# Kernel optimization log

Hardware: AMD Instinct MI355X
Metric: run time of the kernel (lower is better)

## Reference

```python
import jax, jax.numpy as jnp
import numpy as np

# Model dims (match init_kwargs)
B, S = 2, 2048          # batch, seq_len
H = 1024                # hidden_size
D = 2048                # expert_hidden_dim
E = 8                   # num_experts
K = 2                   # num_experts_per_tok (top_k)


def setup_inputs() -> dict:
    key = jax.random.key(0)
    k_x, k_g, k_w1, k_w2 = jax.random.split(key, 4)
    x = jax.random.normal(k_x, (B, S, H), jnp.float32)
    # router gate: Linear(H, E, bias=False)
    gate_w = jax.random.normal(k_g, (H, E), jnp.float32) / jnp.sqrt(H).astype(jnp.float32)
    # per-expert FFN params stacked on leading expert axis
    W1 = jax.random.normal(k_w1, (E, H, D), jnp.float32) / jnp.sqrt(H).astype(jnp.float32)
    b1 = jnp.zeros((E, D), jnp.float32)
    W2 = jax.random.normal(k_w2, (E, D, H), jnp.float32) / jnp.sqrt(D).astype(jnp.float32)
    b2 = jnp.zeros((E, H), jnp.float32)
    return {"x": x, "gate_w": gate_w, "W1": W1, "b1": b1, "W2": W2, "b2": b2}


def reference(x, gate_w, W1, b1, W2, b2):
    # --- router ---
    logits = jnp.einsum('bsh,he->bse', x, gate_w)            # [B,S,E]
    probs = jax.nn.softmax(logits, axis=-1)                  # [B,S,E]
    topk_p, idx = jax.lax.top_k(probs, K)                    # [B,S,K] each
    topk_p = topk_p / topk_p.sum(axis=-1, keepdims=True)     # renormalize over top-k
    one_hot = jax.nn.one_hot(idx, E, dtype=probs.dtype)      # [B,S,K,E]
    # combine weight per (token, expert); topk indices are distinct so this
    # equals the original's masked-sum of router_probs_flat * expert_mask
    combine = jnp.einsum('bske,bsk->bse', one_hot, topk_p)   # [B,S,E]

    # --- aux load-balancing loss (faithful to original reductions) ---
    tokens_per_expert = one_hot.sum(axis=-2).mean(axis=0)    # [S,E]
    avg_prob_per_expert = probs.mean(axis=(0, 1))            # [E]
    aux_loss = E * (tokens_per_expert * avg_prob_per_expert).sum()

    # --- experts: dense-equivalent of gather-FFN-scatter (tokens with
    # combine weight 0 contribute 0, matching the masked loop) ---
    out = jnp.zeros_like(x)
    for e in range(E):  # fixed small loop over structurally distinct experts
        h = jax.nn.gelu(jnp.einsum('bsh,hd->bsd', x, W1[e]) + b1[e], approximate=False)
        out = out + combine[..., e:e + 1] * (jnp.einsum('bsd,dh->bsh', h, W2[e]) + b2[e])
    return out, aux_loss
```

## Files before the change

### kernel.cpp

```cpp
#include <hip/hip_runtime.h>
#include <hip/hip_bf16.h>

#define NTOK 4096
#define HD   1024
#define DD   2048
#define NE   8
#define SLOTS (2*NTOK)

typedef unsigned short u16;
typedef unsigned int   u32;
typedef unsigned long long u64;
typedef __attribute__((ext_vector_type(8))) __bf16 bf16x8;
typedef __attribute__((ext_vector_type(4))) float  f32x4;

__device__ __forceinline__ float bf2f(u16 u) {
    u32 v = ((u32)u) << 16;
    return __uint_as_float(v);
}
__device__ __forceinline__ u16 f2bf(float f) {
    __hip_bfloat16 h = __float2bfloat16(f);
    return *reinterpret_cast<u16*>(&h);
}

__device__ __forceinline__ void gload_lds16(const void* g, void* l) {
    __builtin_amdgcn_global_load_lds(
        (__attribute__((address_space(1))) void*)g,
        (__attribute__((address_space(3))) void*)l,
        16, 0, 0);
}

__device__ __forceinline__ float gelu_f(float v) {
    float x = 0.7978845608028654f * (v + 0.044715f * v * v * v);
    float e = exp2f(x * 2.8853900817779268f);
    float th = 1.f - 2.f * __builtin_amdgcn_rcpf(e + 1.f);
    return 0.5f * v * (1.f + th);
}

__global__ __launch_bounds__(256) void cvtT3_k(
        const float* __restrict__ W1, const float* __restrict__ W2,
        u16* __restrict__ W1t, u16* __restrict__ W2t) {
    int z = blockIdx.z;
    const float* src; u16* dst; int R, C;
    if (z < NE) { src = W1 + (size_t)z * HD * DD;        dst = W1t + (size_t)z * HD * DD;        R = HD; C = DD; }
    else        { src = W2 + (size_t)(z - NE) * DD * HD; dst = W2t + (size_t)(z - NE) * DD * HD; R = DD; C = HD; }
    int ntc = C >> 6;
    int k0  = (blockIdx.x / ntc) * 128;
    int c0  = (blockIdx.x % ntc) * 64;

    __shared__ u16 tt[64 * 136];
    int tid = threadIdx.x;
#pragma unroll
    for (int p = 0; p < 2; ++p) {
        int b  = p * 256 + tid;
        int nq = b & 15;
        int kq = b >> 4;
        float4 v[4];
#pragma unroll
        for (int i = 0; i < 4; ++i)
            v[i] = *reinterpret_cast<const float4*>(
                src + (size_t)(k0 + kq * 4 + i) * C + c0 + nq * 4);
        const float* vf = reinterpret_cast<const float*>(v);
#pragma unroll
        for (int j = 0; j < 4; ++j) {
            int n = nq * 4 + j;
            u16 q4[4] = {f2bf(vf[0 * 4 + j]), f2bf(vf[1 * 4 + j]),
                         f2bf(vf[2 * 4 + j]), f2bf(vf[3 * 4 + j])};
            *reinterpret_cast<u64*>(&tt[n * 136 + kq * 4]) =
                *reinterpret_cast<u64*>(q4);
        }
    }
    __syncthreads();
    int nr = tid >> 4;
    int ch = tid & 15;
#pragma unroll
    for (int p = 0; p < 4; ++p) {
        int n = p * 16 + nr;
        uint4 q = *reinterpret_cast<const uint4*>(&tt[n * 136 + ch * 8]);
        *reinterpret_cast<uint4*>(dst + (size_t)(c0 + n) * R + k0 + ch * 8) = q;
    }
}

__global__ __launch_bounds__(256) void router_k(
        const float* __restrict__ x, const float* __restrict__ gw,
        u16* __restrict__ xb,
        int* __restrict__ counts, float* __restrict__ sum_probs,
        int* __restrict__ tk_idx, float* __restrict__ tk_w) {
    __shared__ int   bcnt[NE];
    __shared__ float bprob[NE];
    int tid = threadIdx.x;
    if (tid < NE) { bcnt[tid] = 0; bprob[tid] = 0.f; }
    __syncthreads();

    int gtid = blockIdx.x * 256 + tid;
    int t    = gtid >> 6;
    int lane = gtid & 63;

    float acc[NE] = {0.f,0.f,0.f,0.f,0.f,0.f,0.f,0.f};
    const float* xr = x + (size_t)t * HD;
    u16* xbr = xb + (size_t)t * HD;
#pragma unroll
    for (int i = 0; i < 4; ++i) {
        int h0 = lane * 4 + i * 256;
        float4 xv4 = *reinterpret_cast<const float4*>(xr + h0);
        u16 xq[4] = {f2bf(xv4.x), f2bf(xv4.y), f2bf(xv4.z), f2bf(xv4.w)};
        *reinterpret_cast<u64*>(xbr + h0) = *reinterpret_cast<u64*>(xq);
        const float xs[4] = {xv4.x, xv4.y, xv4.z, xv4.w};
#pragma unroll
        for (int j = 0; j < 4; ++j) {
            const float4* g = reinterpret_cast<const float4*>(gw + (size_t)(h0 + j) * NE);
            float4 g0 = g[0], g1 = g[1];
            float xv = xs[j];
            acc[0] = fmaf(xv, g0.x, acc[0]); acc[1] = fmaf(xv, g0.y, acc[1]);
            acc[2] = fmaf(xv, g0.z, acc[2]); acc[3] = fmaf(xv, g0.w, acc[3]);
            acc[4] = fmaf(xv, g1.x, acc[4]); acc[5] = fmaf(xv, g1.y, acc[5]);
            acc[6] = fmaf(xv, g1.z, acc[6]); acc[7] = fmaf(xv, g1.w, acc[7]);
        }
    }
#pragma unroll
    for (int off = 32; off >= 1; off >>= 1) {
#pragma unroll
        for (int e = 0; e < NE; ++e) acc[e] += __shfl_xor(acc[e], off);
    }
    float m = acc[0];
#pragma unroll
    for (int e = 1; e < NE; ++e) m = fmaxf(m, acc[e]);
    float p[NE]; float s = 0.f;
#pragma unroll
    for (int e = 0; e < NE; ++e) { p[e] = expf(acc[e] - m); s += p[e]; }
    float inv = 1.f / s;

    int i1 = 0; float v1 = p[0];
#pragma unroll
    for (int e = 1; e < NE; ++e) if (p[e] > v1) { v1 = p[e]; i1 = e; }
    int i2 = -1; float v2 = -1.f;
#pragma unroll
    for (int e = 0; e < NE; ++e) if (e != i1 && p[e] > v2) { v2 = p[e]; i2 = e; }
    float wsum = v1 + v2;

    if (lane < NE) atomicAdd(&bprob[lane], p[lane] * inv);
    if (lane == 0) {
        atomicAdd(&bcnt[i1], 1);
        atomicAdd(&bcnt[i2], 1);
        tk_idx[2 * t]     = i1;  tk_idx[2 * t + 1] = i2;
        tk_w[2 * t]       = v1 / wsum;
        tk_w[2 * t + 1]   = v2 / wsum;
    }
    __syncthreads();
    if (tid < NE) {
        if (bcnt[tid]) atomicAdd(&counts[tid], bcnt[tid]);
        atomicAdd(&sum_probs[tid], bprob[tid]);
    }
}

__global__ __launch_bounds__(256) void scatter_k(
        const int* __restrict__ tk_idx, const int* __restrict__ counts,
        int* __restrict__ cursor, int* __restrict__ slot_tok,
        int* __restrict__ inv_slot, int* __restrict__ offsets) {
    __shared__ int off[NE];
    if (threadIdx.x == 0) {
        int o = 0;
        for (int e = 0; e < NE; ++e) { off[e] = o; o += counts[e]; }
        if (blockIdx.x == 0)
            for (int e = 0; e < NE; ++e) offsets[e] = off[e];
    }
    __syncthreads();
    int t = blockIdx.x * 256 + threadIdx.x;
    if (t >= NTOK) return;
#pragma unroll
    for (int k = 0; k < 2; ++k) {
        int e = tk_idx[2 * t + k];
        int pos = atomicAdd(&cursor[e], 1);
        int s = off[e] + pos;
        slot_tok[s] = t;
        inv_slot[2 * t + k] = s;
    }
}

template<int KD, bool GATHER, bool GELU>
__global__ __launch_bounds__(256) void gemm_dense_k(
        const u16* __restrict__ A,
        const u16* __restrict__ Bt,
        const float* __restrict__ bias,
        const int* __restrict__ counts, const int* __restrict__ offsets,
        const int* __restrict__ slot_tok,
        u16* __restrict__ outb, int ND) {
    int xcd = blockIdx.x & 7;
    int s   = blockIdx.x >> 3;
    int mb  = xcd * 9 + (s >> 4);
    int nx  = s & 15;
    int e = -1, m0 = 0, accb = 0;
#pragma unroll
    for (int ee = 0; ee < NE; ++ee) {
        int nb = (counts[ee] + 127) >> 7;
        if (e < 0 && mb < accb + nb) { e = ee; m0 = (mb - accb) * 128; }
        accb += nb;
    }
    if (e < 0) return;
    int cnt = counts[e], base = offsets[e];
    int n0 = nx * 128;

    __shared__ u16 As[128 * 64];
    __shared__ u16 Bs[128 * 64];
    __shared__ int ids[128];

    int tid  = threadIdx.x;
    int lane = tid & 63;
    int w    = tid >> 6;
    int wr   = w >> 1, wc = w & 1;
    int lrow = lane & 15, khi = lane >> 4;

    if constexpr (GATHER) {
        if (tid < 128) ids[tid] = (m0 + tid < cnt) ? slot_tok[base + m0 + tid] : 0;
    }
    __syncthreads();

    const u16* Bte = Bt + (size_t)e * (size_t)ND * KD;
    int srow = tid >> 3;
    int sslot = tid & 7;

    const u16 *gA[4], *gB[4];
#pragma unroll
    for (int j = 0; j < 4; ++j) {
        int r = j * 32 + srow;
        size_t gr;
        if constexpr (GATHER) gr = (size_t)ids[r];
        else                  gr = (size_t)(base + m0 + r);
        gA[j] = A   + gr * KD                + ((sslot ^ (r & 7)) << 3);
        gB[j] = Bte + (size_t)(n0 + r) * KD  + ((sslot ^ (r & 7)) << 3);
    }

    f32x4 acc[4][4];
#pragma unroll
    for (int m = 0; m < 4; ++m)
#pragma unroll
        for (int n = 0; n < 4; ++n) acc[m][n] = {0.f, 0.f, 0.f, 0.f};

    constexpr int NK = KD / 64;
#pragma unroll 1
    for (int t = 0; t < NK; ++t) {
#pragma unroll
        for (int j = 0; j < 4; ++j) {
            gload_lds16(gA[j] + t * 64, (char*)As + j * 4096 + tid * 16);
            gload_lds16(gB[j] + t * 64, (char*)Bs + j * 4096 + tid * 16);
        }
        __syncthreads();
#pragma unroll
        for (int ks = 0; ks < 2; ++ks) {
            int slot = ks * 4 + khi;
            bf16x8 af[4], bv[4];
#pragma unroll
            for (int m = 0; m < 4; ++m) {
                int r = wr * 64 + m * 16 + lrow;
                af[m] = *reinterpret_cast<const bf16x8*>(
                    &As[r * 64 + ((slot ^ (r & 7)) << 3)]);
            }
#pragma unroll
            for (int n = 0; n < 4; ++n) {
                int r = wc * 64 + n * 16 + lrow;
                bv[n] = *reinterpret_cast<const bf16x8*>(
                    &Bs[r * 64 + ((slot ^ (r & 7)) << 3)]);
            }
            __builtin_amdgcn_s_setprio(1);
#pragma unroll
            for (int m = 0; m < 4; ++m)
#pragma unroll
                for (int n = 0; n < 4; ++n)
                    acc[m][n] = __builtin_amdgcn_mfma_f32_16x16x32_bf16(
                        af[m], bv[n], acc[m][n], 0, 0, 0);
            __builtin_amdgcn_s_setprio(0);
        }
        __syncthreads();
    }

    constexpr int PST = 72;
    u16* patch = As + w * 16 * PST;
    float bvals[4];
    if constexpr (GELU) {
#pragma unroll
        for (int n = 0; n < 4; ++n)
            bvals[n] = bias[(size_t)e * ND + n0 + wc * 64 + n * 16 + lrow];
    }
#pragma unroll
    for (int m = 0; m < 4; ++m) {
#pragma unroll
        for (int n = 0; n < 4; ++n)
#pragma unroll
            for (int i = 0; i < 4; ++i) {
                float v = acc[m][n][i];
                if constexpr (GELU) {
                    v += bvals[n];
                    v = gelu_f(v);
                }
                patch[(khi * 4 + i) * PST + n * 16 + lrow] = f2bf(v);
            }
        __syncthreads();
        int prow = lane >> 3, sl = lane & 7;
#pragma unroll
        for (int p = 0; p < 2; ++p) {
            int row  = p * 8 + prow;
            uint4 q = *reinterpret_cast<const uint4*>(&patch[row * PST + sl * 8]);
            int grow = m0 + wr * 64 + m * 16 + row;
            if (grow < cnt)
                *reinterpret_cast<uint4*>(
                    outb + (size_t)(base + grow) * ND + n0 + wc * 64 + sl * 8) = q;
        }
        __syncthreads();
    }
}

template<int KD>
__global__ __launch_bounds__(256) void gemm_n64_k(
        const u16* __restrict__ A,
        const u16* __restrict__ Bt,
        const int* __restrict__ counts, const int* __restrict__ offsets,
        u16* __restrict__ outb, int ND) {
    int xcd = blockIdx.x & 7;
    int s   = blockIdx.x >> 3;
    int mb  = xcd * 9 + (s >> 4);
    int nx  = s & 15;
    int e = -1, m0 = 0, accb = 0;
#pragma unroll
    for (int ee = 0; ee < NE; ++ee) {
        int nb = (counts[ee] + 127) >> 7;
        if (e < 0 && mb < accb + nb) { e = ee; m0 = (mb - accb) * 128; }
        accb += nb;
    }
    if (e < 0) return;
    int cnt = counts[e], base = offsets[e];
    int n0 = nx * 64;

    __shared__ u16 As[128 * 64];
    __shared__ u16 Bs[64 * 64];

    int tid  = threadIdx.x;
    int lane = tid & 63;
    int w    = tid >> 6;
    int wr   = w >> 1, wc = w & 1;
    int lrow = lane & 15, khi = lane >> 4;

    const u16* Bte = Bt + (size_t)e * (size_t)ND * KD;
    int srow = tid >> 3;
    int sslot = tid & 7;

    const u16 *gA[4], *gB[2];
#pragma unroll
    for (int j = 0; j < 4; ++j) {
        int r = j * 32 + srow;
        gA[j] = A + (size_t)(base + m0 + r) * KD + ((sslot ^ (r & 7)) << 3);
    }
#pragma unroll
    for (int j = 0; j < 2; ++j) {
        int r = j * 32 + srow;
        gB[j] = Bte + (size_t)(n0 + r) * KD + ((sslot ^ (r & 7)) << 3);
    }

    f32x4 acc[4][2];
#pragma unroll
    for (int m = 0; m < 4; ++m)
#pragma unroll
        for (int n = 0; n < 2; ++n) acc[m][n] = {0.f, 0.f, 0.f, 0.f};

    constexpr int NK = KD / 64;
#pragma unroll 1
    for (int t = 0; t < NK; ++t) {
#pragma unroll
        for (int j = 0; j < 4; ++j)
            gload_lds16(gA[j] + t * 64, (char*)As + j * 4096 + tid * 16);
#pragma unroll
        for (int j = 0; j < 2; ++j)
            gload_lds16(gB[j] + t * 64, (char*)Bs + j * 4096 + tid * 16);
        __syncthreads();
#pragma unroll
        for (int ks = 0; ks < 2; ++ks) {
            int slot = ks * 4 + khi;
            bf16x8 af[4], bv[2];
#pragma unroll
            for (int m = 0; m < 4; ++m) {
                int r = wr * 64 + m * 16 + lrow;
                af[m] = *reinterpret_cast<const bf16x8*>(
                    &As[r * 64 + ((slot ^ (r & 7)) << 3)]);
            }
#pragma unroll
            for (int n = 0; n < 2; ++n) {
                int r = wc * 32 + n * 16 + lrow;
                bv[n] = *reinterpret_cast<const bf16x8*>(
                    &Bs[r * 64 + ((slot ^ (r & 7)) << 3)]);
            }
            __builtin_amdgcn_s_setprio(1);
#pragma unroll
            for (int m = 0; m < 4; ++m)
#pragma unroll
                for (int n = 0; n < 2; ++n)
                    acc[m][n] = __builtin_amdgcn_mfma_f32_16x16x32_bf16(
                        af[m], bv[n], acc[m][n], 0, 0, 0);
            __builtin_amdgcn_s_setprio(0);
        }
        __syncthreads();
    }

    constexpr int PST = 40;
    u16* patch = As + w * 16 * PST;
#pragma unroll
    for (int m = 0; m < 4; ++m) {
#pragma unroll
        for (int n = 0; n < 2; ++n)
#pragma unroll
            for (int i = 0; i < 4; ++i)
                patch[(khi * 4 + i) * PST + n * 16 + lrow] = f2bf(acc[m][n][i]);
        __syncthreads();
        int row = lane >> 2, sl = lane & 3;
        uint4 q = *reinterpret_cast<const uint4*>(&patch[row * PST + sl * 8]);
        int grow = m0 + wr * 64 + m * 16 + row;
        if (grow < cnt)
            *reinterpret_cast<uint4*>(
                outb + (size_t)(base + grow) * ND + n0 + wc * 32 + sl * 8) = q;
        __syncthreads();
    }
}

__global__ __launch_bounds__(256) void combine_k(
        const int* __restrict__ tk_idx, const float* __restrict__ tk_w,
        const int* __restrict__ inv_slot, const u16* __restrict__ ybuf,
        const float* __restrict__ b2, float* __restrict__ out,
        const int* __restrict__ counts, const float* __restrict__ sum_probs,
        float* __restrict__ out_aux) {
    if (blockIdx.x == 0 && threadIdx.x == 0) {
        double s = 0.0;
        for (int e = 0; e < NE; ++e) s += (double)counts[e] * (double)sum_probs[e];
        out_aux[0] = (float)(s * (8.0 / (2.0 * (double)NTOK)));
    }
    int gtid = blockIdx.x * 256 + threadIdx.x;
    int t = gtid >> 6;
    int lane = gtid & 63;
    int e0 = tk_idx[2 * t], e1 = tk_idx[2 * t + 1];
    float w0 = tk_w[2 * t], w1 = tk_w[2 * t + 1];
    int s0 = inv_slot[2 * t], s1 = inv_slot[2 * t + 1];

#pragma unroll
    for (int i = 0; i < 2; ++i) {
        int c = lane * 8 + i * 512;
        uint4 q0 = *reinterpret_cast<const uint4*>(ybuf + (size_t)s0 * HD + c);
        uint4 q1 = *reinterpret_cast<const uint4*>(ybuf + (size_t)s1 * HD + c);
        float y0[8] = {bf2f((u16)(q0.x&0xffff)), bf2f((u16)(q0.x>>16)),
                       bf2f((u16)(q0.y&0xffff)), bf2f((u16)(q0.y>>16)),
                       bf2f((u16)(q0.z&0xffff)), bf2f((u16)(q0.z>>16)),
                       bf2f((u16)(q0.w&0xffff)), bf2f((u16)(q0.w>>16))};
        float y1[8] = {bf2f((u16)(q1.x&0xffff)), bf2f((u16)(q1.x>>16)),
                       bf2f((u16)(q1.y&0xffff)), bf2f((u16)(q1.y>>16)),
                       bf2f((u16)(q1.z&0xffff)), bf2f((u16)(q1.z>>16)),
                       bf2f((u16)(q1.w&0xffff)), bf2f((u16)(q1.w>>16))};
        float r[8];
#pragma unroll
        for (int j = 0; j < 8; ++j) {
            float v0 = y0[j] + b2[e0 * HD + c + j];
            float v1 = y1[j] + b2[e1 * HD + c + j];
            r[j] = w0 * v0 + w1 * v1;
        }
        float* op = out + (size_t)t * HD + c;
        *reinterpret_cast<float4*>(op)     = make_float4(r[0], r[1], r[2], r[3]);
        *reinterpret_cast<float4*>(op + 4) = make_float4(r[4], r[5], r[6], r[7]);
    }
}

extern "C" void kernel_launch(void* const* d_in, const int* in_sizes, int n_in,
                              void* d_out, int out_size, void* d_ws, size_t ws_size,
                              hipStream_t stream) {
    const float* x   = (const float*)d_in[0];
    const float* gw  = (const float*)d_in[1];
    const float* W1  = (const float*)d_in[2];
    const float* b1  = (const float*)d_in[3];
    const float* W2  = (const float*)d_in[4];
    const float* b2  = (const float*)d_in[5];
    float* out = (float*)d_out;

    char* ws = (char*)d_ws;
    int*   counts    = (int*)(ws + 0);
    int*   cursor    = (int*)(ws + 32);
    int*   offsets   = (int*)(ws + 64);
    float* sum_probs = (float*)(ws + 128);
    int*   tk_idx    = (int*)(ws + 512);
    float* tk_w      = (float*)(ws + 33280);
    int*   slot_tok  = (int*)(ws + 66048);
    int*   inv_slot  = (int*)(ws + 98816);
    u16*   xb        = (u16*)(ws + 131584);
    u16*   W1t       = (u16*)(ws + 8520192);
    u16*   W2t       = (u16*)(ws + 42074624);
    u16*   hbuf      = (u16*)(ws + 75629056);
    u16*   ybuf      = W1t;

    hipMemsetAsync(ws, 0, 512, stream);

    cvtT3_k<<<dim3(256, 1, 2 * NE), 256, 0, stream>>>(W1, W2, W1t, W2t);
    router_k<<<NTOK / 4, 256, 0, stream>>>(x, gw, xb, counts, sum_probs, tk_idx, tk_w);
    scatter_k<<<NTOK / 256, 256, 0, stream>>>(tk_idx, counts, cursor,
                                              slot_tok, inv_slot, offsets);

    gemm_dense_k<HD, true, true><<<1152, 256, 0, stream>>>(
        xb, W1t, b1, counts, offsets, slot_tok, hbuf, DD);
    gemm_n64_k<DD><<<1152, 256, 0, stream>>>(
        hbuf, W2t, counts, offsets, ybuf, HD);

    combine_k<<<NTOK / 4, 256, 0, stream>>>(tk_idx, tk_w, inv_slot, ybuf, b2, out,
                                            counts, sum_probs,
                                            out + (size_t)NTOK * HD);
}
```

Before: 211.9 us.

## Fuse weight conversion into router and GEMM1 launches to overlap work

Splits the W1/W2 fp32-to-bf16 transpose: W1 conversion is merged into the router launch as extra blocks, and W2 conversion runs as extra blocks appended to the first expert GEMM launch. This removes separate kernel launches and lets the memory-bound conversion overlap with router and GEMM1 compute. The conversion tile also moves to 8 rows per thread with 16-byte LDS stores. The risk is that conversion blocks compete with GEMM blocks for CUs and bandwidth, and that block ordering decides how much real overlap happens.

```diff
diff --git a/kernel.cpp b/kernel.cpp
--- a/kernel.cpp
+++ b/kernel.cpp
@@ -36,42 +36,27 @@
     return 0.5f * v * (1.f + th);
 }
 
-__global__ __launch_bounds__(256) void cvtT3_k(
-        const float* __restrict__ W1, const float* __restrict__ W2,
-        u16* __restrict__ W1t, u16* __restrict__ W2t) {
-    int z = blockIdx.z;
-    const float* src; u16* dst; int R, C;
-    if (z < NE) { src = W1 + (size_t)z * HD * DD;        dst = W1t + (size_t)z * HD * DD;        R = HD; C = DD; }
-    else        { src = W2 + (size_t)(z - NE) * DD * HD; dst = W2t + (size_t)(z - NE) * DD * HD; R = DD; C = HD; }
-    int ntc = C >> 6;
-    int k0  = (blockIdx.x / ntc) * 128;
-    int c0  = (blockIdx.x % ntc) * 64;
-
-    __shared__ u16 tt[64 * 136];
-    int tid = threadIdx.x;
-#pragma unroll
-    for (int p = 0; p < 2; ++p) {
-        int b  = p * 256 + tid;
-        int nq = b & 15;
-        int kq = b >> 4;
-        float4 v[4];
-#pragma unroll
-        for (int i = 0; i < 4; ++i)
-            v[i] = *reinterpret_cast<const float4*>(
-                src + (size_t)(k0 + kq * 4 + i) * C + c0 + nq * 4);
-        const float* vf = reinterpret_cast<const float*>(v);
-#pragma unroll
-        for (int j = 0; j < 4; ++j) {
-            int n = nq * 4 + j;
-            u16 q4[4] = {f2bf(vf[0 * 4 + j]), f2bf(vf[1 * 4 + j]),
-                         f2bf(vf[2 * 4 + j]), f2bf(vf[3 * 4 + j])};
-            *reinterpret_cast<u64*>(&tt[n * 136 + kq * 4]) =
-                *reinterpret_cast<u64*>(q4);
-        }
+__device__ __forceinline__ void cvt_tile(const float* __restrict__ src,
+                                         u16* __restrict__ dst,
+                                         int R, int C, int k0, int c0,
+                                         u16* tt, int tid) {
+    int kg = tid >> 4, ng = tid & 15;
+    float4 v[8];
+#pragma unroll
+    for (int i = 0; i < 8; ++i)
+        v[i] = *reinterpret_cast<const float4*>(
+            src + (size_t)(k0 + kg * 8 + i) * C + c0 + ng * 4);
+    const float* vf = reinterpret_cast<const float*>(v);
+#pragma unroll
+    for (int j = 0; j < 4; ++j) {
+        u16 q8[8];
+#pragma unroll
+        for (int i = 0; i < 8; ++i) q8[i] = f2bf(vf[i * 4 + j]);
+        *reinterpret_cast<uint4*>(&tt[(ng * 4 + j) * 136 + kg * 8]) =
+            *reinterpret_cast<uint4*>(q8);
     }
     __syncthreads();
-    int nr = tid >> 4;
-    int ch = tid & 15;
+    int nr = tid >> 4, ch = tid & 15;
 #pragma unroll
     for (int p = 0; p < 4; ++p) {
         int n = p * 16 + nr;
@@ -80,18 +65,30 @@
     }
 }
 
-__global__ __launch_bounds__(256) void router_k(
+__global__ __launch_bounds__(256) void prep1_k(
+        const float* __restrict__ W1, u16* __restrict__ W1t,
         const float* __restrict__ x, const float* __restrict__ gw,
         u16* __restrict__ xb,
         int* __restrict__ counts, float* __restrict__ sum_probs,
         int* __restrict__ tk_idx, float* __restrict__ tk_w) {
-    __shared__ int   bcnt[NE];
-    __shared__ float bprob[NE];
+    __shared__ __align__(16) u16 tt[64 * 136];
+    int bid = blockIdx.x;
     int tid = threadIdx.x;
+    if (bid < 2048) {
+        int z  = bid >> 8;
+        int xq = bid & 255;
+        int k0 = (xq >> 5) * 128;
+        int c0 = (xq & 31) * 64;
+        cvt_tile(W1 + (size_t)z * HD * DD, W1t + (size_t)z * HD * DD,
+                 HD, DD, k0, c0, tt, tid);
+        return;
+    }
+    int*   bcnt  = reinterpret_cast<int*>(tt);
+    float* bprob = reinterpret_cast<float*>(tt + 32);
     if (tid < NE) { bcnt[tid] = 0; bprob[tid] = 0.f; }
     __syncthreads();
 
-    int gtid = blockIdx.x * 256 + tid;
+    int gtid = (bid - 2048) * 256 + tid;
     int t    = gtid >> 6;
     int lane = gtid & 63;
 
@@ -176,14 +173,33 @@
     }
 }
 
-template<int KD, bool GATHER, bool GELU>
-__global__ __launch_bounds__(256) void gemm_dense_k(
+__global__ __launch_bounds__(256) void gemm1cvt_k(
         const u16* __restrict__ A,
         const u16* __restrict__ Bt,
         const float* __restrict__ bias,
         const int* __restrict__ counts, const int* __restrict__ offsets,
         const int* __restrict__ slot_tok,
-        u16* __restrict__ outb, int ND) {
+        u16* __restrict__ outb,
+        const float* __restrict__ W2, u16* __restrict__ W2t) {
+    __shared__ __align__(16) char smraw[33280];
+    int tid = threadIdx.x;
+
+    if (blockIdx.x >= 1152) {
+        int cb = blockIdx.x - 1152;
+        int z  = cb >> 8;
+        int xq = cb & 255;
+        int k0 = (xq >> 4) * 128;
+        int c0 = (xq & 15) * 64;
+        cvt_tile(W2 + (size_t)z * DD * HD, W2t + (size_t)z * DD * HD,
+                 DD, HD, k0, c0, (u16*)smraw, tid);
+        return;
+    }
+
+    constexpr int KD = HD, ND = DD;
+    u16* As = (u16*)smraw;
+    u16* Bs = As + 128 * 64;
+    int* ids = (int*)(Bs + 128 * 64);
+
     int xcd = blockIdx.x & 7;
     int s   = blockIdx.x >> 3;
     int mb  = xcd * 9 + (s >> 4);
@@ -199,19 +215,12 @@
     int cnt = counts[e], base = offsets[e];
     int n0 = nx * 128;
 
-    __shared__ u16 As[128 * 64];
-    __shared__ u16 Bs[128 * 64];
-    __shared__ int ids[128];
-
-    int tid  = threadIdx.x;
     int lane = tid & 63;
     int w    = tid >> 6;
     int wr   = w >> 1, wc = w & 1;
     int lrow = lane & 15, khi = lane >> 4;
 
-    if constexpr (GATHER) {
-        if (tid < 128) ids[tid] = (m0 + tid < cnt) ? slot_tok[base + m0 + tid] : 0;
-    }
+    if (tid < 128) ids[tid] = (m0 + tid < cnt) ? slot_tok[base + m0 + tid] : 0;
     __syncthreads();
 
     const u16* Bte = Bt + (size_t)e * (size_t)ND * KD;
@@ -222,10 +231,7 @@
 #pragma unroll
     for (int j = 0; j < 4; ++j) {
         int r = j * 32 + srow;
-        size_t gr;
-        if constexpr (GATHER) gr = (size_t)ids[r];
-        else                  gr = (size_t)(base + m0 + r);
-        gA[j] = A   + gr * KD                + ((sslot ^ (r & 7)) << 3);
+        gA[j] = A   + (size_t)ids[r] * KD    + ((sslot ^ (r & 7)) << 3);
         gB[j] = Bte + (size_t)(n0 + r) * KD  + ((sslot ^ (r & 7)) << 3);
     }
 
@@ -275,22 +281,17 @@
     constexpr int PST = 72;
     u16* patch = As + w * 16 * PST;
     float bvals[4];
-    if constexpr (GELU) {
+#pragma unroll
+    for (int n = 0; n < 4; ++n)
+        bvals[n] = bias[(size_t)e * ND + n0 + wc * 64 + n * 16 + lrow];
+#pragma unroll
+    for (int m = 0; m < 4; ++m) {
 #pragma unroll
         for (int n = 0; n < 4; ++n)
-            bvals[n] = bias[(size_t)e * ND + n0 + wc * 64 + n * 16 + lrow];
-    }
-#pragma unroll
-    for (int m = 0; m < 4; ++m) {
-#pragma unroll
-        for (int n = 0; n < 4; ++n)
 #pragma unroll
             for (int i = 0; i < 4; ++i) {
-                float v = acc[m][n][i];
-                if constexpr (GELU) {
-                    v += bvals[n];
-                    v = gelu_f(v);
-                }
+                float v = acc[m][n][i] + bvals[n];
+                v = gelu_f(v);
                 patch[(khi * 4 + i) * PST + n * 16 + lrow] = f2bf(v);
             }
         __syncthreads();
@@ -490,13 +491,13 @@
 
     hipMemsetAsync(ws, 0, 512, stream);
 
-    cvtT3_k<<<dim3(256, 1, 2 * NE), 256, 0, stream>>>(W1, W2, W1t, W2t);
-    router_k<<<NTOK / 4, 256, 0, stream>>>(x, gw, xb, counts, sum_probs, tk_idx, tk_w);
+    prep1_k<<<2048 + 1024, 256, 0, stream>>>(W1, W1t, x, gw, xb,
+                                             counts, sum_probs, tk_idx, tk_w);
     scatter_k<<<NTOK / 256, 256, 0, stream>>>(tk_idx, counts, cursor,
                                               slot_tok, inv_slot, offsets);
 
-    gemm_dense_k<HD, true, true><<<1152, 256, 0, stream>>>(
-        xb, W1t, b1, counts, offsets, slot_tok, hbuf, DD);
+    gemm1cvt_k<<<1152 + 2048, 256, 0, stream>>>(
+        xb, W1t, b1, counts, offsets, slot_tok, hbuf, W2, W2t);
     gemm_n64_k<DD><<<1152, 256, 0, stream>>>(
         hbuf, W2t, counts, offsets, ybuf, HD);
 
```

Result: faster. 202.0 us (-4.7%).
